# Kernel tuning notes

Hardware: AMD Instinct MI355X
Metric: run time of the kernel (lower is better)

## Reference

```python
import jax, jax.numpy as jnp
import numpy as np

T_KD = 20.0      # KL_divergence temperature
T_THR = 6.0      # Threshold_weights temperature
EPS = 1e-05


def _margin(o, gathered):
    # torch.sort descending, take top-2; margin only when target is the argmax value
    top2 = jax.lax.top_k(o, 2)[0]                      # [B, 2]
    return jnp.where(top2[:, 0] == gathered, top2[:, 0] - top2[:, 1], 0.0)


def _forward(outputs1, outputs2, outputs3, outputs4, out_s, targets):
    B = targets.shape[0]
    idx = jnp.arange(B)
    mimic = (outputs1 + outputs2 + outputs3 + outputs4) / 4.0

    teachers = [outputs1, outputs2, outputs3, outputs4, mimic]
    gathered = [t[idx, targets] for t in teachers]      # each [B]

    # C = min over gathered target logits of the 4 real teachers
    C = jnp.minimum(jnp.minimum(gathered[0].min(), gathered[1].min()),
                    jnp.minimum(gathered[2].min(), gathered[3].min()))
    # if C < 0: shift everything by (-C + eps); else no shift
    shift = jnp.where(C < 0, -C + EPS, 0.0)

    shifted = [t + shift for t in teachers]
    g_shift = [g + shift for g in gathered]

    # Threshold_weights: margin per branch, softmax over 5 branches
    preds = jnp.stack([_margin(s, g) for s, g in zip(shifted, g_shift)], axis=1)  # [B,5]
    out_threshold = jax.nn.softmax(preds / T_THR, axis=1)

    # max over the 4 (shifted) teacher logit tensors
    max_preds = jnp.maximum(jnp.maximum(shifted[0].max(), shifted[1].max()),
                            jnp.maximum(shifted[2].max(), shifted[3].max()))

    # per-sample CE of student (shared across branches)
    log_p_s = jax.nn.log_softmax(out_s, axis=1)
    CE = -log_p_s[idx, targets]                          # [B]

    log_ps_T = jax.nn.log_softmax(out_s / T_KD, axis=1)  # [B,C]

    def branch_loss(teacher, g_s):
        w2 = g_s / max_preds          # weights2
        w1 = 1.0 - w2                 # weights1
        log_pt = jax.nn.log_softmax(teacher / T_KD, axis=1)
        p_t = jnp.exp(log_pt)
        KD = jnp.sum(p_t * (log_pt - log_ps_T), axis=1) * (T_KD * T_KD)  # [B]
        return w1 * CE + w2 * KD

    # KD/CE use the ORIGINAL (unshifted) teacher logits
    losses = jnp.stack([branch_loss(t, g) for t, g in zip(teachers, g_shift)], axis=1)  # [B,5]
    return jnp.mean(jnp.sum(out_threshold * losses, axis=1))


def setup_inputs() -> dict:
    key = jax.random.key(0)
    ks = jax.random.split(key, 6)
    B, C = 8192, 1000
    return {
        "outputs1": jax.random.normal(ks[0], (B, C), dtype=jnp.float32),
        "outputs2": jax.random.normal(ks[1], (B, C), dtype=jnp.float32),
        "outputs3": jax.random.normal(ks[2], (B, C), dtype=jnp.float32),
        "outputs4": jax.random.normal(ks[3], (B, C), dtype=jnp.float32),
        "out_s": jax.random.normal(ks[4], (B, C), dtype=jnp.float32),
        "targets": jax.random.randint(ks[5], (B,), 0, C, dtype=jnp.int64 if jax.config.jax_enable_x64 else jnp.int32),
    }


def reference(outputs1, outputs2, outputs3, outputs4, out_s, targets):
    return _forward(outputs1, outputs2, outputs3, outputs4, out_s, targets)
```

## Files before the change

### kernel.cpp

```cpp
#include <hip/hip_runtime.h>
#include <math.h>

#define NB 8192
#define NC 1000
#define NF4 250


#define LOG2E 1.4426950408889634f
#define LN2   0.6931471805599453f

__device__ __forceinline__ float fexp2(float x) { return __builtin_amdgcn_exp2f(x); }
__device__ __forceinline__ float flog2(float x) { return __builtin_amdgcn_logf(x); }

template <int CTRL>
__device__ __forceinline__ float dpp_mov(float v, float ident) {
  return __uint_as_float((unsigned)__builtin_amdgcn_update_dpp(
      (int)__float_as_uint(ident), (int)__float_as_uint(v), CTRL, 0xF, 0xF,
      false));
}

__device__ __forceinline__ float dppredsum(float v) {
  v += dpp_mov<0x111>(v, 0.f);
  v += dpp_mov<0x112>(v, 0.f);
  v += dpp_mov<0x114>(v, 0.f);
  v += dpp_mov<0x118>(v, 0.f);
  v += dpp_mov<0x142>(v, 0.f);
  v += dpp_mov<0x143>(v, 0.f);
  return v;
}

__device__ __forceinline__ void dppredtop2(float& t1, float& t2) {
  const float NI = -INFINITY;
#define T2STEP(C)                                   \
  {                                                 \
    float i1 = dpp_mov<C>(t1, NI);                  \
    float i2 = dpp_mov<C>(t2, NI);                  \
    t2 = fmaxf(fmaxf(t2, i2), fminf(t1, i1));       \
    t1 = fmaxf(t1, i1);                             \
  }
  T2STEP(0x111) T2STEP(0x112) T2STEP(0x114) T2STEP(0x118)
  T2STEP(0x142) T2STEP(0x143)
#undef T2STEP
}

__device__ __forceinline__ float wredsum(float v) {
#pragma unroll
  for (int m = 32; m >= 1; m >>= 1) v += __shfl_xor(v, m, 64);
  return v;
}
__device__ __forceinline__ float wredmax(float v) {
#pragma unroll
  for (int m = 32; m >= 1; m >>= 1) v = fmaxf(v, __shfl_xor(v, m, 64));
  return v;
}
__device__ __forceinline__ float wredmin(float v) {
#pragma unroll
  for (int m = 32; m >= 1; m >>= 1) v = fminf(v, __shfl_xor(v, m, 64));
  return v;
}
__device__ __forceinline__ float f4get(const float4& v, int e) {
  return e == 0 ? v.x : e == 1 ? v.y : e == 2 ? v.z : v.w;
}

__global__ __launch_bounds__(256) void k_rowstats(
    const float* __restrict__ o1, const float* __restrict__ o2,
    const float* __restrict__ o3, const float* __restrict__ o4,
    const float* __restrict__ os, const int* __restrict__ tg,
    float* __restrict__ ws) {
  const int lane = threadIdx.x & 63;
  const int wv = threadIdx.x >> 6;
  const int row = blockIdx.x;
  const size_t base = (size_t)row * NC;
  const int f = (threadIdx.x < NF4) ? (int)threadIdx.x : 0;
  const bool act = threadIdx.x < NF4;

  float g1 = 0.f, g2 = 0.f, g3 = 0.f, g4 = 0.f, gs = 0.f;
  if (wv == 0) {
    const int target = tg[row];
    g1 = o1[base + target];
    g2 = o2[base + target];
    g3 = o3[base + target];
    g4 = o4[base + target];
    gs = os[base + target];
  }

  const float4 c1 = ((const float4*)(o1 + base))[f];
  const float4 c2 = ((const float4*)(o2 + base))[f];
  const float4 c3 = ((const float4*)(o3 + base))[f];
  const float4 c4 = ((const float4*)(o4 + base))[f];
  const float4 cs = ((const float4*)(os + base))[f];

  float t1[5], t2[5], Z[5], S1[5];
#pragma unroll
  for (int t = 0; t < 5; ++t) {
    t1[t] = -INFINITY; t2[t] = -INFINITY; Z[t] = 0.f; S1[t] = 0.f;
  }
  float Z1 = 0.f, Z20 = 0.f;
  const float K20 = LOG2E / 20.0f;

  if (act) {
#pragma unroll
    for (int e = 0; e < 4; ++e) {
      float w0 = f4get(c1, e);
      float w1 = f4get(c2, e);
      float w2 = f4get(c3, e);
      float w3 = f4get(c4, e);
      float wsv = f4get(cs, e);
      float wm = ((w0 + w1) + w2 + w3) * 0.25f;
      float w[5] = {w0, w1, w2, w3, wm};
#pragma unroll
      for (int t = 0; t < 5; ++t) {
        t2[t] = fmaxf(t2[t], fminf(t1[t], w[t]));
        t1[t] = fmaxf(t1[t], w[t]);
        float et = fexp2(w[t] * K20);
        Z[t] += et;
        S1[t] = fmaf(et, w[t] - wsv, S1[t]);
      }
      Z1 += fexp2(wsv * LOG2E);
      Z20 += fexp2(wsv * K20);
    }
  }

#pragma unroll
  for (int t = 0; t < 5; ++t) dppredtop2(t1[t], t2[t]);
#pragma unroll
  for (int t = 0; t < 5; ++t) { Z[t] = dppredsum(Z[t]); S1[t] = dppredsum(S1[t]); }
  Z1 = dppredsum(Z1);
  Z20 = dppredsum(Z20);

  __shared__ float sred[4][22];
  if (lane == 63) {
#pragma unroll
    for (int t = 0; t < 5; ++t) {
      sred[wv][t] = t1[t];
      sred[wv][5 + t] = t2[t];
      sred[wv][10 + t] = Z[t];
      sred[wv][15 + t] = S1[t];
    }
    sred[wv][20] = Z1;
    sred[wv][21] = Z20;
  }
  __syncthreads();

  if (threadIdx.x == 0) {
    float T1[5], T2[5], ZZ[5], SS[5], z1, z20;
#pragma unroll
    for (int t = 0; t < 5; ++t) {
      T1[t] = sred[0][t]; T2[t] = sred[0][5 + t];
      ZZ[t] = sred[0][10 + t]; SS[t] = sred[0][15 + t];
    }
    z1 = sred[0][20]; z20 = sred[0][21];
#pragma unroll
    for (int w = 1; w < 4; ++w) {
#pragma unroll
      for (int t = 0; t < 5; ++t) {
        float a1 = sred[w][t], a2 = sred[w][5 + t];
        float lo = fminf(T1[t], a1);
        T1[t] = fmaxf(T1[t], a1);
        T2[t] = fmaxf(fmaxf(T2[t], a2), lo);
        ZZ[t] += sred[w][10 + t];
        SS[t] += sred[w][15 + t];
      }
      z1 += sred[w][20];
      z20 += sred[w][21];
    }

    const float gm = ((g1 + g2) + g3 + g4) * 0.25f;
    float gg[5] = {g1, g2, g3, g4, gm};

    const float lse_s = flog2(z20) * LN2;
    const float CE = flog2(z1) * LN2 - gs;

#pragma unroll
    for (int t = 0; t < 5; ++t) {
      float lse_t = flog2(ZZ[t]) * LN2;
      float KD = 400.0f * (SS[t] / (20.0f * ZZ[t]) - lse_t + lse_s);
      float margin = (T1[t] == gg[t]) ? (T1[t] - T2[t]) : 0.0f;
      ws[(size_t)t * NB + row] = margin;
      ws[(size_t)(5 + t) * NB + row] = gg[t];
      ws[(size_t)(10 + t) * NB + row] = KD;
    }
    ws[(size_t)15 * NB + row] = CE;
    ws[(size_t)16 * NB + row] = fminf(fminf(g1, g2), fminf(g3, g4));
    ws[(size_t)17 * NB + row] = fmaxf(fmaxf(T1[0], T1[1]), fmaxf(T1[2], T1[3]));
  }
}

__global__ __launch_bounds__(1024) void k_minmax(float* __restrict__ ws,
                                                 float* __restrict__ out) {
  const int tid = threadIdx.x;
  const int lane = tid & 63, wv = tid >> 6;
  __shared__ float sA[16], sB[16];

  float mn = INFINITY, mx = -INFINITY;
  for (int r = tid; r < NB; r += 1024) {
    mn = fminf(mn, ws[(size_t)16 * NB + r]);
    mx = fmaxf(mx, ws[(size_t)17 * NB + r]);
  }
  mn = wredmin(mn);
  mx = wredmax(mx);
  if (lane == 0) { sA[wv] = mn; sB[wv] = mx; }
  __syncthreads();
  if (tid == 0) {
    float a = sA[0], b = sB[0];
    for (int i = 1; i < 16; ++i) { a = fminf(a, sA[i]); b = fmaxf(b, sB[i]); }
    float shift = (a < 0.0f) ? (-a + 1e-5f) : 0.0f;
    ws[(size_t)18 * NB] = shift;
    ws[(size_t)18 * NB + 1] = b + shift;
    out[0] = 0.0f;
  }
}

__global__ __launch_bounds__(256) void k_loss(const float* __restrict__ ws,
                                              float* __restrict__ out) {
  const int tid = threadIdx.x;
  const int lane = tid & 63, wv = tid >> 6;
  const int r = blockIdx.x * 256 + tid;
  __shared__ float sA[4];

  const float shift = ws[(size_t)18 * NB];
  const float maxp = ws[(size_t)18 * NB + 1];
  const float K6 = LOG2E / 6.0f;

  float m[5], e[5];
#pragma unroll
  for (int t = 0; t < 5; ++t) m[t] = ws[(size_t)t * NB + r];
  float pm = fmaxf(fmaxf(fmaxf(m[0], m[1]), fmaxf(m[2], m[3])), m[4]);
  float Zl = 0.0f;
#pragma unroll
  for (int t = 0; t < 5; ++t) { e[t] = fexp2((m[t] - pm) * K6); Zl += e[t]; }
  float ce = ws[(size_t)15 * NB + r];
  float rl = 0.0f;
#pragma unroll
  for (int t = 0; t < 5; ++t) {
    float g = ws[(size_t)(5 + t) * NB + r];
    float kd = ws[(size_t)(10 + t) * NB + r];
    float w2 = (g + shift) / maxp;
    float loss = (1.0f - w2) * ce + w2 * kd;
    rl += e[t] * loss;
  }
  float acc = rl / Zl;

  acc = wredsum(acc);
  if (lane == 0) sA[wv] = acc;
  __syncthreads();
  if (tid == 0) {
    float tot = (sA[0] + sA[1]) + (sA[2] + sA[3]);
    atomicAdd(out, tot * (1.0f / 8192.0f));
  }
}

extern "C" void kernel_launch(void* const* d_in, const int* in_sizes, int n_in,
                              void* d_out, int out_size, void* d_ws, size_t ws_size,
                              hipStream_t stream) {
  const float* o1 = (const float*)d_in[0];
  const float* o2 = (const float*)d_in[1];
  const float* o3 = (const float*)d_in[2];
  const float* o4 = (const float*)d_in[3];
  const float* os = (const float*)d_in[4];
  const int* tg = (const int*)d_in[5];
  float* ws = (float*)d_ws;
  float* out = (float*)d_out;

  k_rowstats<<<NB, 256, 0, stream>>>(o1, o2, o3, o4, os, tg, ws);
  k_minmax<<<1, 1024, 0, stream>>>(ws, out);
  k_loss<<<NB / 256, 256, 0, stream>>>(ws, out);
}
```

Before: 191.6 us.

## Map one row per wavefront and fuse min/max reduction into loss kernel

The row-stats kernel now assigns one row to each 64-lane wavefront, looping four times over float4 chunks, instead of one row per 256-thread block. This removes the shared-memory cross-wave reduction and the block barrier, and uses all lanes rather than leaving six idle. The separate single-block min/max kernel is folded into the loss kernel: every block redundantly recomputes the global min/max over 8192 values, which removes one launch. The output zeroing moves into the first kernel. In exchange, each wave issues its loads serially across iterations, and each loss block re-reads 64KB of workspace.

Result: slower. 199.2 us (+4.0%).

```diff
diff --git a/kernel.cpp b/kernel.cpp
--- a/kernel.cpp
+++ b/kernel.cpp
@@ -62,33 +62,17 @@
   return e == 0 ? v.x : e == 1 ? v.y : e == 2 ? v.z : v.w;
 }
 
-__global__ __launch_bounds__(256) void k_rowstats(
+__global__ __launch_bounds__(256, 8) void k_rowstats(
     const float* __restrict__ o1, const float* __restrict__ o2,
     const float* __restrict__ o3, const float* __restrict__ o4,
     const float* __restrict__ os, const int* __restrict__ tg,
-    float* __restrict__ ws) {
+    float* __restrict__ ws, float* __restrict__ out) {
   const int lane = threadIdx.x & 63;
   const int wv = threadIdx.x >> 6;
-  const int row = blockIdx.x;
+  const int row = (blockIdx.x << 2) + wv;
   const size_t base = (size_t)row * NC;
-  const int f = (threadIdx.x < NF4) ? (int)threadIdx.x : 0;
-  const bool act = threadIdx.x < NF4;
-
-  float g1 = 0.f, g2 = 0.f, g3 = 0.f, g4 = 0.f, gs = 0.f;
-  if (wv == 0) {
-    const int target = tg[row];
-    g1 = o1[base + target];
-    g2 = o2[base + target];
-    g3 = o3[base + target];
-    g4 = o4[base + target];
-    gs = os[base + target];
-  }
-
-  const float4 c1 = ((const float4*)(o1 + base))[f];
-  const float4 c2 = ((const float4*)(o2 + base))[f];
-  const float4 c3 = ((const float4*)(o3 + base))[f];
-  const float4 c4 = ((const float4*)(o4 + base))[f];
-  const float4 cs = ((const float4*)(os + base))[f];
+
+  if (blockIdx.x == 0 && threadIdx.x == 0) out[0] = 0.0f;
 
   float t1[5], t2[5], Z[5], S1[5];
 #pragma unroll
@@ -98,28 +82,44 @@
   float Z1 = 0.f, Z20 = 0.f;
   const float K20 = LOG2E / 20.0f;
 
-  if (act) {
-#pragma unroll
-    for (int e = 0; e < 4; ++e) {
-      float w0 = f4get(c1, e);
-      float w1 = f4get(c2, e);
-      float w2 = f4get(c3, e);
-      float w3 = f4get(c4, e);
-      float wsv = f4get(cs, e);
-      float wm = ((w0 + w1) + w2 + w3) * 0.25f;
-      float w[5] = {w0, w1, w2, w3, wm};
-#pragma unroll
-      for (int t = 0; t < 5; ++t) {
-        t2[t] = fmaxf(t2[t], fminf(t1[t], w[t]));
-        t1[t] = fmaxf(t1[t], w[t]);
-        float et = fexp2(w[t] * K20);
-        Z[t] += et;
-        S1[t] = fmaf(et, w[t] - wsv, S1[t]);
+#pragma unroll 1
+  for (int i = 0; i < 4; ++i) {
+    const int f = lane + (i << 6);
+    if (f < NF4) {
+      const float4 c1 = ((const float4*)(o1 + base))[f];
+      const float4 c2 = ((const float4*)(o2 + base))[f];
+      const float4 c3 = ((const float4*)(o3 + base))[f];
+      const float4 c4 = ((const float4*)(o4 + base))[f];
+      const float4 cs = ((const float4*)(os + base))[f];
+#pragma unroll
+      for (int e = 0; e < 4; ++e) {
+        float w0 = f4get(c1, e);
+        float w1 = f4get(c2, e);
+        float w2 = f4get(c3, e);
+        float w3 = f4get(c4, e);
+        float wsv = f4get(cs, e);
+        float wm = ((w0 + w1) + w2 + w3) * 0.25f;
+        float w[5] = {w0, w1, w2, w3, wm};
+#pragma unroll
+        for (int t = 0; t < 5; ++t) {
+          t2[t] = fmaxf(t2[t], fminf(t1[t], w[t]));
+          t1[t] = fmaxf(t1[t], w[t]);
+          float et = fexp2(w[t] * K20);
+          Z[t] += et;
+          S1[t] = fmaf(et, w[t] - wsv, S1[t]);
+        }
+        Z1 += fexp2(wsv * LOG2E);
+        Z20 += fexp2(wsv * K20);
       }
-      Z1 += fexp2(wsv * LOG2E);
-      Z20 += fexp2(wsv * K20);
     }
   }
+
+  const int target = tg[row];
+  const float g1 = o1[base + target];
+  const float g2 = o2[base + target];
+  const float g3 = o3[base + target];
+  const float g4 = o4[base + target];
+  const float gs = os[base + target];
 
 #pragma unroll
   for (int t = 0; t < 5; ++t) dppredtop2(t1[t], t2[t]);
@@ -128,98 +128,54 @@
   Z1 = dppredsum(Z1);
   Z20 = dppredsum(Z20);
 
-  __shared__ float sred[4][22];
   if (lane == 63) {
-#pragma unroll
-    for (int t = 0; t < 5; ++t) {
-      sred[wv][t] = t1[t];
-      sred[wv][5 + t] = t2[t];
-      sred[wv][10 + t] = Z[t];
-      sred[wv][15 + t] = S1[t];
-    }
-    sred[wv][20] = Z1;
-    sred[wv][21] = Z20;
-  }
-  __syncthreads();
-
-  if (threadIdx.x == 0) {
-    float T1[5], T2[5], ZZ[5], SS[5], z1, z20;
-#pragma unroll
-    for (int t = 0; t < 5; ++t) {
-      T1[t] = sred[0][t]; T2[t] = sred[0][5 + t];
-      ZZ[t] = sred[0][10 + t]; SS[t] = sred[0][15 + t];
-    }
-    z1 = sred[0][20]; z20 = sred[0][21];
-#pragma unroll
-    for (int w = 1; w < 4; ++w) {
-#pragma unroll
-      for (int t = 0; t < 5; ++t) {
-        float a1 = sred[w][t], a2 = sred[w][5 + t];
-        float lo = fminf(T1[t], a1);
-        T1[t] = fmaxf(T1[t], a1);
-        T2[t] = fmaxf(fmaxf(T2[t], a2), lo);
-        ZZ[t] += sred[w][10 + t];
-        SS[t] += sred[w][15 + t];
-      }
-      z1 += sred[w][20];
-      z20 += sred[w][21];
-    }
-
     const float gm = ((g1 + g2) + g3 + g4) * 0.25f;
     float gg[5] = {g1, g2, g3, g4, gm};
 
-    const float lse_s = flog2(z20) * LN2;
-    const float CE = flog2(z1) * LN2 - gs;
+    const float lse_s = flog2(Z20) * LN2;
+    const float CE = flog2(Z1) * LN2 - gs;
 
 #pragma unroll
     for (int t = 0; t < 5; ++t) {
-      float lse_t = flog2(ZZ[t]) * LN2;
-      float KD = 400.0f * (SS[t] / (20.0f * ZZ[t]) - lse_t + lse_s);
-      float margin = (T1[t] == gg[t]) ? (T1[t] - T2[t]) : 0.0f;
+      float lse_t = flog2(Z[t]) * LN2;
+      float KD = 400.0f * (S1[t] / (20.0f * Z[t]) - lse_t + lse_s);
+      float margin = (t1[t] == gg[t]) ? (t1[t] - t2[t]) : 0.0f;
       ws[(size_t)t * NB + row] = margin;
       ws[(size_t)(5 + t) * NB + row] = gg[t];
       ws[(size_t)(10 + t) * NB + row] = KD;
     }
     ws[(size_t)15 * NB + row] = CE;
     ws[(size_t)16 * NB + row] = fminf(fminf(g1, g2), fminf(g3, g4));
-    ws[(size_t)17 * NB + row] = fmaxf(fmaxf(T1[0], T1[1]), fmaxf(T1[2], T1[3]));
-  }
-}
-
-__global__ __launch_bounds__(1024) void k_minmax(float* __restrict__ ws,
-                                                 float* __restrict__ out) {
+    ws[(size_t)17 * NB + row] = fmaxf(fmaxf(t1[0], t1[1]), fmaxf(t1[2], t1[3]));
+  }
+}
+
+__global__ __launch_bounds__(256) void k_final(const float* __restrict__ ws,
+                                               float* __restrict__ out) {
   const int tid = threadIdx.x;
   const int lane = tid & 63, wv = tid >> 6;
-  __shared__ float sA[16], sB[16];
+  __shared__ float sMn[4], sMx[4], sA[4];
 
   float mn = INFINITY, mx = -INFINITY;
-  for (int r = tid; r < NB; r += 1024) {
-    mn = fminf(mn, ws[(size_t)16 * NB + r]);
-    mx = fmaxf(mx, ws[(size_t)17 * NB + r]);
+  const float4* mnp = (const float4*)(ws + (size_t)16 * NB);
+  const float4* mxp = (const float4*)(ws + (size_t)17 * NB);
+#pragma unroll 1
+  for (int r4 = tid; r4 < NB / 4; r4 += 256) {
+    float4 a = mnp[r4];
+    float4 b = mxp[r4];
+    mn = fminf(mn, fminf(fminf(a.x, a.y), fminf(a.z, a.w)));
+    mx = fmaxf(mx, fmaxf(fmaxf(b.x, b.y), fmaxf(b.z, b.w)));
   }
   mn = wredmin(mn);
   mx = wredmax(mx);
-  if (lane == 0) { sA[wv] = mn; sB[wv] = mx; }
+  if (lane == 0) { sMn[wv] = mn; sMx[wv] = mx; }
   __syncthreads();
-  if (tid == 0) {
-    float a = sA[0], b = sB[0];
-    for (int i = 1; i < 16; ++i) { a = fminf(a, sA[i]); b = fmaxf(b, sB[i]); }
-    float shift = (a < 0.0f) ? (-a + 1e-5f) : 0.0f;
-    ws[(size_t)18 * NB] = shift;
-    ws[(size_t)18 * NB + 1] = b + shift;
-    out[0] = 0.0f;
-  }
-}
-
-__global__ __launch_bounds__(256) void k_loss(const float* __restrict__ ws,
-                                              float* __restrict__ out) {
-  const int tid = threadIdx.x;
-  const int lane = tid & 63, wv = tid >> 6;
+  const float a = fminf(fminf(sMn[0], sMn[1]), fminf(sMn[2], sMn[3]));
+  const float b = fmaxf(fmaxf(sMx[0], sMx[1]), fmaxf(sMx[2], sMx[3]));
+  const float shift = (a < 0.0f) ? (-a + 1e-5f) : 0.0f;
+  const float maxp = b + shift;
+
   const int r = blockIdx.x * 256 + tid;
-  __shared__ float sA[4];
-
-  const float shift = ws[(size_t)18 * NB];
-  const float maxp = ws[(size_t)18 * NB + 1];
   const float K6 = LOG2E / 6.0f;
 
   float m[5], e[5];
@@ -262,7 +218,6 @@
   float* ws = (float*)d_ws;
   float* out = (float*)d_out;
 
-  k_rowstats<<<NB, 256, 0, stream>>>(o1, o2, o3, o4, os, tg, ws);
-  k_minmax<<<1, 1024, 0, stream>>>(ws, out);
-  k_loss<<<NB / 256, 256, 0, stream>>>(ws, out);
-}
+  k_rowstats<<<NB / 4, 256, 0, stream>>>(o1, o2, o3, o4, os, tg, ws, out);
+  k_final<<<NB / 256, 256, 0, stream>>>(ws, out);
+}
```
